# Kernel tuning notes

Hardware: AMD Instinct MI355X
Metric: run time of the kernel (lower is better)

Reference implementation:

```python
import jax, jax.numpy as jnp
import numpy as np

SIGMA_NEU = 0.05
SIGMA_SYN = 0.002
JIJ_STD = 0.045


def setup_inputs() -> dict:
    key = jax.random.key(0)
    ks = jax.random.split(key, 6)
    B, T, n_in, n_hid, n_out = 64, 64, 128, 256, 32
    input_signal = jax.random.normal(ks[0], (B, T, n_in), dtype=jnp.float32)
    hidden = jax.random.normal(ks[1], (B, n_hid), dtype=jnp.float32)
    # nn.Linear default init approximated by scaled normals; w_hh uses uniform(-jij_std, jij_std)
    w_in_w = jax.random.normal(ks[2], (n_hid, n_in), dtype=jnp.float32) / np.sqrt(n_in)
    w_hh_w = jax.random.uniform(ks[3], (n_hid, n_hid), minval=-JIJ_STD, maxval=JIJ_STD, dtype=jnp.float32)
    w_hh_b = jnp.zeros((n_hid,), dtype=jnp.float32)
    w_out_w = jax.random.normal(ks[4], (n_out, n_hid), dtype=jnp.float32) / np.sqrt(n_hid)
    alpha = jnp.full((n_hid,), 0.25, dtype=jnp.float32)
    beta = jnp.full((n_hid,), 0.1, dtype=jnp.float32)
    return {
        "input_signal": input_signal,
        "hidden": hidden,
        "length": T,
        "w_in_w": w_in_w,
        "w_hh_w": w_hh_w,
        "w_hh_b": w_hh_b,
        "w_out_w": w_out_w,
        "alpha": alpha,
        "beta": beta,
    }


def reference(input_signal, hidden, length, w_in_w, w_hh_w, w_hh_b, w_out_w, alpha, beta):
    # tanh activation, beta != 0 branch, anti-Hebbian plasticity.
    B, T, n_in = input_signal.shape
    n_hid = hidden.shape[1]
    x = jnp.transpose(input_signal, (1, 0, 2))  # (T, B, n_in)
    keys = jax.random.split(jax.random.key(42), length)
    sqrt_alpha = jnp.sqrt(alpha)
    sqrt_beta = jnp.sqrt(beta)
    # Track only different_j = new_j - w_hh (starts at 0); new_j never needed separately.
    diff_j0 = jnp.zeros((B, n_hid, n_hid), dtype=input_signal.dtype)

    def step(carry, inp):
        h, diff_j = carry
        xt, k = inp
        k1, k2 = jax.random.split(k)
        act = jnp.tanh(h)
        # row-vector times per-sample fast-weight matrix: (b,1,n) @ (b,n,n) -> (b,n)
        dj_act = jnp.einsum('bi,bij->bj', act, diff_j)
        tmp = xt @ w_in_w.T + act @ w_hh_w.T + w_hh_b + dj_act
        neural_noise = jax.random.normal(k1, h.shape, h.dtype) * SIGMA_NEU * sqrt_alpha
        h = (1.0 - alpha) * h + alpha * tmp + neural_noise
        # anti-Hebbian: -outer(act, act) + syn noise (sqrt(beta) broadcasts on last dim)
        add_w = -jnp.einsum('bi,bj->bij', act, act) \
                + jax.random.normal(k2, diff_j.shape, diff_j.dtype) * SIGMA_SYN * sqrt_beta
        diff_j = diff_j + beta * add_w
        out = 20.0 * jnp.tanh(h @ w_out_w.T)
        return (h, diff_j), (h, out)

    (hidden, _), (h_seq, o_seq) = jax.lax.scan(step, (hidden, diff_j0), (x, keys))
    hidden_list = jnp.transpose(h_seq, (1, 0, 2))  # (B, T, n_hid)
    output_list = jnp.transpose(o_seq, (1, 0, 2))  # (B, T, n_out)
    return hidden_list, output_list, hidden
```

## Files before the change

kernel.cpp:

```cpp
#include <hip/hip_runtime.h>
#include <stdint.h>

#define BB 64
#define TT 64
#define NIN 128
#define NHID 256
#define NOUT 32
#define BPS 16
#define NBLK (BB * BPS)
#define NTHR 256
#define JS 16

#define SIG_NEU 0.05f
#define SIG_SYN 0.002f

#define FLAG_OFF    0
#define FLAG_STRIDE 32
#define FLAG_BYTES  (BB * BPS * FLAG_STRIDE * 4)
#define HPUB_OFF    FLAG_BYTES

#define HID_LIST_SZ ((size_t)BB * TT * NHID)
#define OUT_LIST_SZ ((size_t)BB * TT * NOUT)

__device__ __forceinline__ uint32_t rotl32(uint32_t v, int s) {
  return __builtin_amdgcn_alignbit(v, v, 32 - s);
}

__device__ __forceinline__ void tf2x32(uint32_t k0, uint32_t k1, uint32_t x0, uint32_t x1,
                                       uint32_t& o0, uint32_t& o1) {
  const uint32_t k2 = k0 ^ k1 ^ 0x1BD11BDAu;
  x0 += k0; x1 += k1;
  x0 += x1; x1 = rotl32(x1,13); x1 ^= x0;
  x0 += x1; x1 = rotl32(x1,15); x1 ^= x0;
  x0 += x1; x1 = rotl32(x1,26); x1 ^= x0;
  x0 += x1; x1 = rotl32(x1, 6); x1 ^= x0;
  x0 += k1; x1 += k2 + 1u;
  x0 += x1; x1 = rotl32(x1,17); x1 ^= x0;
  x0 += x1; x1 = rotl32(x1,29); x1 ^= x0;
  x0 += x1; x1 = rotl32(x1,16); x1 ^= x0;
  x0 += x1; x1 = rotl32(x1,24); x1 ^= x0;
  x0 += k2; x1 += k0 + 2u;
  x0 += x1; x1 = rotl32(x1,13); x1 ^= x0;
  x0 += x1; x1 = rotl32(x1,15); x1 ^= x0;
  x0 += x1; x1 = rotl32(x1,26); x1 ^= x0;
  x0 += x1; x1 = rotl32(x1, 6); x1 ^= x0;
  x0 += k0; x1 += k1 + 3u;
  x0 += x1; x1 = rotl32(x1,17); x1 ^= x0;
  x0 += x1; x1 = rotl32(x1,29); x1 ^= x0;
  x0 += x1; x1 = rotl32(x1,16); x1 ^= x0;
  x0 += x1; x1 = rotl32(x1,24); x1 ^= x0;
  x0 += k1; x1 += k2 + 4u;
  x0 += x1; x1 = rotl32(x1,13); x1 ^= x0;
  x0 += x1; x1 = rotl32(x1,15); x1 ^= x0;
  x0 += x1; x1 = rotl32(x1,26); x1 ^= x0;
  x0 += x1; x1 = rotl32(x1, 6); x1 ^= x0;
  x0 += k2; x1 += k0 + 5u;
  o0 = x0; o1 = x1;
}

__device__ __forceinline__ float tf_normal(uint32_t k0, uint32_t k1, uint32_t idx) {
  uint32_t o0, o1;
  tf2x32(k0, k1, 0u, idx, o0, o1);
  const uint32_t bits = o0 ^ o1;
  const float u = __uint_as_float((bits >> 9) | 0x3f800000u) - 1.0f;
  float x = fmaf(u, 2.0f, -0.99999994f);
  x = fmaxf(x, -0.99999994f);
  const float w = -__logf(fmaf(-x, x, 1.0f));
  float p;
  if (w < 5.0f) {
    const float q = w - 2.5f;
    p = 2.81022636e-08f;
    p = fmaf(p, q, 3.43273939e-07f);
    p = fmaf(p, q, -3.5233877e-06f);
    p = fmaf(p, q, -4.39150654e-06f);
    p = fmaf(p, q, 0.00021858087f);
    p = fmaf(p, q, -0.00125372503f);
    p = fmaf(p, q, -0.00417768164f);
    p = fmaf(p, q, 0.246640727f);
    p = fmaf(p, q, 1.50140941f);
  } else {
    const float q = sqrtf(w) - 3.0f;
    p = -0.000200214257f;
    p = fmaf(p, q, 0.000100950558f);
    p = fmaf(p, q, 0.00134934322f);
    p = fmaf(p, q, -0.00367342844f);
    p = fmaf(p, q, 0.00573950773f);
    p = fmaf(p, q, -0.0076224613f);
    p = fmaf(p, q, 0.00943887047f);
    p = fmaf(p, q, 1.00167406f);
    p = fmaf(p, q, 2.83297682f);
  }
  return 1.41421356f * (p * x);
}

#define SPIN(slice, want)                                                         \
  do {                                                                            \
    uint32_t* fp_ = &flags[((b) * BPS + (slice)) * FLAG_STRIDE];                  \
    for (int it_ = 0; it_ < 2000000; ++it_) {                                     \
      if (__hip_atomic_load(fp_, __ATOMIC_RELAXED, __HIP_MEMORY_SCOPE_AGENT) >=   \
          (uint32_t)(want)) break;                                                \
      __builtin_amdgcn_s_sleep(1);                                                \
    }                                                                             \
  } while (0)

__global__ __launch_bounds__(NTHR, 4)
void rnn_kernel(
    const float* __restrict__ xin, const float* __restrict__ h0,
    const float* __restrict__ w_in, const float* __restrict__ w_hh,
    const float* __restrict__ b_hh, const float* __restrict__ w_out,
    const float* __restrict__ alpha, const float* __restrict__ beta,
    float* __restrict__ out, char* __restrict__ ws)
{
  __shared__ __align__(16) float whh_s[JS * 260];
  __shared__ __align__(16) float win_s[JS * 132];
  __shared__ __align__(16) float wos[2 * 260];
  __shared__ __align__(16) float h_s[NHID];
  __shared__ __align__(16) float a_s[NHID];
  __shared__ __align__(16) float xt_s[NIN];
  __shared__ float stat_s[JS];
  __shared__ float djact_s[JS];
  __shared__ uint32_t keys_s[TT * 4];

  const int tid = threadIdx.x;
  const int blk = blockIdx.x;
  const int b   = blk & 63;
  const int s   = blk >> 6;

  uint32_t* flags = (uint32_t*)(ws + FLAG_OFF);
  float*    hpub  = (float*)(ws + HPUB_OFF);

  if (tid < TT) {
    uint32_t ka, kb, t0, t1;
    tf2x32(0u, 42u, 0u, (uint32_t)tid, ka, kb);
    tf2x32(ka, kb, 0u, 0u, t0, t1);
    keys_s[tid * 4 + 0] = t0; keys_s[tid * 4 + 1] = t1;
    tf2x32(ka, kb, 0u, 1u, t0, t1);
    keys_s[tid * 4 + 2] = t0; keys_s[tid * 4 + 3] = t1;
  }
  {
    const float hv = h0[b * NHID + tid];
    h_s[tid] = hv;
    a_s[tid] = tanhf(hv);
  }
  #pragma unroll
  for (int r = 0; r < JS; ++r)
    whh_s[r * 260 + tid] = w_hh[(size_t)(s * JS + r) * NHID + tid];
  {
    const int r2 = tid >> 7, c = tid & 127;
    #pragma unroll
    for (int rr = 0; rr < 8; ++rr)
      win_s[(rr * 2 + r2) * 132 + c] = w_in[(size_t)(s * JS + rr * 2 + r2) * NIN + c];
  }
  #pragma unroll
  for (int r = 0; r < 2; ++r)
    wos[r * 260 + tid] = w_out[(s * 2 + r) * NHID + tid];

  const int q  = tid & 15;
  const int jl = tid >> 4;
  const int jg = s * JS + jl;
  const float bj   = beta[jg];
  const float sbj  = SIG_SYN * sqrtf(bj);
  const float bjsb = bj * sbj;
  const uint32_t idx0 = ((uint32_t)b << 16) | (uint32_t)jg;
  const float bias = b_hh[jg];

  uint32_t idxs[16];
  #pragma unroll
  for (int c4 = 0; c4 < 4; ++c4) {
    const uint32_t rowb = (uint32_t)(q * 16 + ((c4 + q) & 3) * 4);
    #pragma unroll
    for (int cc = 0; cc < 4; ++cc)
      idxs[c4 * 4 + cc] = idx0 + ((rowb + (uint32_t)cc) << 8);
  }

  float r_al = 0.f, r_om = 0.f, r_ns = 0.f;
  uint32_t hnidx = 0;
  if (tid < JS) {
    r_al = alpha[s * JS + tid];
    r_om = 1.0f - r_al;
    r_ns = SIG_NEU * sqrtf(r_al);
    hnidx = (uint32_t)(b * NHID + s * JS + tid);
  }

  float d[16];
  #pragma unroll
  for (int r = 0; r < 16; ++r) d[r] = 0.0f;
  float hn = 0.0f;

  __syncthreads();

  {
    if (tid < JS) {
      const uint32_t k1a = __builtin_amdgcn_readfirstlane(keys_s[0]);
      const uint32_t k1b = __builtin_amdgcn_readfirstlane(keys_s[1]);
      hn = tf_normal(k1a, k1b, hnidx);
    }
    if (tid < NIN) xt_s[tid] = xin[((size_t)b * TT) * NIN + tid];
  }
  __syncthreads();

  const int wv = tid >> 6;
  const int ln = tid & 63;

  for (int t = 0; t < TT; ++t) {
    const int par = t & 1;

    const float aj = a_s[jg];
    float pd = 0.0f;
    float acc = 0.0f;
    #pragma unroll
    for (int c4 = 0; c4 < 4; ++c4) {
      const int col = q * 16 + ((c4 + q) & 3) * 4;
      const float4 av = *(const float4*)(a_s + col);
      const float4 wv4 = *(const float4*)(whh_s + jl * 260 + col);
      pd = fmaf(av.x, d[c4*4+0], pd);
      pd = fmaf(av.y, d[c4*4+1], pd);
      pd = fmaf(av.z, d[c4*4+2], pd);
      pd = fmaf(av.w, d[c4*4+3], pd);
      d[c4*4+0] = fmaf(bj, -av.x * aj, d[c4*4+0]);
      d[c4*4+1] = fmaf(bj, -av.y * aj, d[c4*4+1]);
      d[c4*4+2] = fmaf(bj, -av.z * aj, d[c4*4+2]);
      d[c4*4+3] = fmaf(bj, -av.w * aj, d[c4*4+3]);
      acc = fmaf(wv4.x, av.x, acc); acc = fmaf(wv4.y, av.y, acc);
      acc = fmaf(wv4.z, av.z, acc); acc = fmaf(wv4.w, av.w, acc);
    }
    #pragma unroll
    for (int k = 0; k < 2; ++k) {
      const int col = q * 8 + ((k + q) & 1) * 4;
      const float4 xv = *(const float4*)(xt_s + col);
      const float4 wv4 = *(const float4*)(win_s + jl * 132 + col);
      acc = fmaf(wv4.x, xv.x, acc); acc = fmaf(wv4.y, xv.y, acc);
      acc = fmaf(wv4.z, xv.z, acc); acc = fmaf(wv4.w, xv.w, acc);
    }
    pd  += __shfl_xor(pd, 1);  pd  += __shfl_xor(pd, 2);
    pd  += __shfl_xor(pd, 4);  pd  += __shfl_xor(pd, 8);
    acc += __shfl_xor(acc, 1); acc += __shfl_xor(acc, 2);
    acc += __shfl_xor(acc, 4); acc += __shfl_xor(acc, 8);
    if (q == 0) {
      djact_s[jl] = pd;
      stat_s[jl]  = acc + bias;
    }

    if (wv == 3 && t > 0) {
      const int o = ln >> 5, sub = ln & 31;
      float oacc = 0.0f;
      #pragma unroll
      for (int k = 0; k < 2; ++k) {
        const int col = sub * 8 + ((k + sub) & 1) * 4;
        const float4 wvv = *(const float4*)(wos + o * 260 + col);
        const float4 hv  = *(const float4*)(h_s + col);
        oacc = fmaf(wvv.x, hv.x, oacc); oacc = fmaf(wvv.y, hv.y, oacc);
        oacc = fmaf(wvv.z, hv.z, oacc); oacc = fmaf(wvv.w, hv.w, oacc);
      }
      oacc += __shfl_xor(oacc, 1);  oacc += __shfl_xor(oacc, 2);
      oacc += __shfl_xor(oacc, 4);  oacc += __shfl_xor(oacc, 8);
      oacc += __shfl_xor(oacc, 16);
      if (sub == 0)
        out[HID_LIST_SZ + ((size_t)b * TT + (t - 1)) * NOUT + s * 2 + o] =
            20.0f * tanhf(oacc);
    }
    __syncthreads();

    if (tid < JS) {
      const float tmp  = stat_s[tid] + djact_s[tid];
      const float hnew = fmaf(r_al, tmp, r_om * h_s[s * JS + tid]) + hn * r_ns;
      __hip_atomic_store(&hpub[(par * BB + b) * NHID + s * JS + tid], hnew,
                         __ATOMIC_RELAXED, __HIP_MEMORY_SCOPE_AGENT);
    }
    if (tid == 0) {
      asm volatile("s_waitcnt vmcnt(0)" ::: "memory");
      __hip_atomic_store(&flags[(b * BPS + s) * FLAG_STRIDE], (uint32_t)(t + 1),
                         __ATOMIC_RELAXED, __HIP_MEMORY_SCOPE_AGENT);
    }

    if (t + 1 < TT) {
      const uint32_t k2a = __builtin_amdgcn_readfirstlane(keys_s[t * 4 + 2]);
      const uint32_t k2b = __builtin_amdgcn_readfirstlane(keys_s[t * 4 + 3]);
      #pragma unroll
      for (int e = 0; e < 16; ++e)
        d[e] = fmaf(bjsb, tf_normal(k2a, k2b, idxs[e]), d[e]);
      if (tid < JS) {
        const uint32_t k1a = __builtin_amdgcn_readfirstlane(keys_s[(t + 1) * 4 + 0]);
        const uint32_t k1b = __builtin_amdgcn_readfirstlane(keys_s[(t + 1) * 4 + 1]);
        hn = tf_normal(k1a, k1b, hnidx);
      }
    }

    if (wv == 0) {
      if (ln < BPS) SPIN(ln, t + 1);
      asm volatile("" ::: "memory");
      #pragma unroll
      for (int cc = 0; cc < 4; ++cc) {
        const int k = ln * 4 + cc;
        const float hv = __hip_atomic_load(&hpub[(par * BB + b) * NHID + k],
                                           __ATOMIC_RELAXED, __HIP_MEMORY_SCOPE_AGENT);
        h_s[k] = hv;
        a_s[k] = tanhf(hv);
      }
    } else if (wv == 1) {
      if (s == 0) {
        if (ln < BPS) SPIN(ln, t + 1);
        asm volatile("" ::: "memory");
        #pragma unroll
        for (int cc = 0; cc < 4; ++cc) {
          const int k = ln * 4 + cc;
          const float hv = __hip_atomic_load(&hpub[(par * BB + b) * NHID + k],
                                             __ATOMIC_RELAXED, __HIP_MEMORY_SCOPE_AGENT);
          out[((size_t)b * TT + t) * NHID + k] = hv;
          if (t == TT - 1)
            out[HID_LIST_SZ + OUT_LIST_SZ + (size_t)b * NHID + k] = hv;
        }
      }
    } else if (wv == 2) {
      if (t + 1 < TT) {
        xt_s[ln]      = xin[((size_t)b * TT + t + 1) * NIN + ln];
        xt_s[ln + 64] = xin[((size_t)b * TT + t + 1) * NIN + ln + 64];
      }
    }
    __syncthreads();
  }

  if (wv == 3) {
    const int o = ln >> 5, sub = ln & 31;
    float oacc = 0.0f;
    #pragma unroll
    for (int k = 0; k < 2; ++k) {
      const int col = sub * 8 + ((k + sub) & 1) * 4;
      const float4 wvv = *(const float4*)(wos + o * 260 + col);
      const float4 hv  = *(const float4*)(h_s + col);
      oacc = fmaf(wvv.x, hv.x, oacc); oacc = fmaf(wvv.y, hv.y, oacc);
      oacc = fmaf(wvv.z, hv.z, oacc); oacc = fmaf(wvv.w, hv.w, oacc);
    }
    oacc += __shfl_xor(oacc, 1);  oacc += __shfl_xor(oacc, 2);
    oacc += __shfl_xor(oacc, 4);  oacc += __shfl_xor(oacc, 8);
    oacc += __shfl_xor(oacc, 16);
    if (sub == 0)
      out[HID_LIST_SZ + ((size_t)b * TT + (TT - 1)) * NOUT + s * 2 + o] =
          20.0f * tanhf(oacc);
  }
}

extern "C" void kernel_launch(void* const* d_in, const int* in_sizes, int n_in,
                              void* d_out, int out_size, void* d_ws, size_t ws_size,
                              hipStream_t stream) {
  (void)in_sizes; (void)n_in; (void)out_size; (void)ws_size;
  const float* x     = (const float*)d_in[0];
  const float* h0    = (const float*)d_in[1];
  const float* w_in  = (const float*)d_in[3];
  const float* w_hh  = (const float*)d_in[4];
  const float* b_hh  = (const float*)d_in[5];
  const float* w_out = (const float*)d_in[6];
  const float* alpha = (const float*)d_in[7];
  const float* beta  = (const float*)d_in[8];
  float* out = (float*)d_out;

  hipMemsetAsync((char*)d_ws + FLAG_OFF, 0, FLAG_BYTES, stream);
  rnn_kernel<<<dim3(NBLK), dim3(NTHR), 0, stream>>>(
      x, h0, w_in, w_hh, b_hh, w_out, alpha, beta, out, (char*)d_ws);
}
```

Before: 816.7 us.

## Split each batch row across 32 blocks with 8 hidden units per block

Doubles the number of cooperating blocks per batch sample from 16 to 32, halving the hidden rows each block owns (JS 16→8). Each thread now holds 8 fast-weight entries instead of 16 and generates half as many synaptic-noise normals per step, with 32-lane reductions and strided float2 column access. This cuts per-block per-step compute and register pressure (launch bounds raised to 8 blocks/SM), at the cost of twice as many flags to spin on and more cross-block synchronisation traffic per timestep. The 2048 blocks must all be co-resident for the spin-wait scheme to avoid deadlock.

```diff
diff --git a/kernel.cpp b/kernel.cpp
--- a/kernel.cpp
+++ b/kernel.cpp
@@ -6,10 +6,10 @@
 #define NIN 128
 #define NHID 256
 #define NOUT 32
-#define BPS 16
+#define BPS 32
 #define NBLK (BB * BPS)
 #define NTHR 256
-#define JS 16
+#define JS 8
 
 #define SIG_NEU 0.05f
 #define SIG_SYN 0.002f
@@ -103,7 +103,7 @@
     }                                                                             \
   } while (0)
 
-__global__ __launch_bounds__(NTHR, 4)
+__global__ __launch_bounds__(NTHR, 8)
 void rnn_kernel(
     const float* __restrict__ xin, const float* __restrict__ h0,
     const float* __restrict__ w_in, const float* __restrict__ w_hh,
@@ -111,9 +111,9 @@
     const float* __restrict__ alpha, const float* __restrict__ beta,
     float* __restrict__ out, char* __restrict__ ws)
 {
-  __shared__ __align__(16) float whh_s[JS * 260];
-  __shared__ __align__(16) float win_s[JS * 132];
-  __shared__ __align__(16) float wos[2 * 260];
+  __shared__ __align__(16) float whh_s[JS * NHID];
+  __shared__ __align__(16) float win_s[JS * NIN];
+  __shared__ __align__(16) float wos_s[NHID];
   __shared__ __align__(16) float h_s[NHID];
   __shared__ __align__(16) float a_s[NHID];
   __shared__ __align__(16) float xt_s[NIN];
@@ -144,19 +144,14 @@
   }
   #pragma unroll
   for (int r = 0; r < JS; ++r)
-    whh_s[r * 260 + tid] = w_hh[(size_t)(s * JS + r) * NHID + tid];
-  {
-    const int r2 = tid >> 7, c = tid & 127;
-    #pragma unroll
-    for (int rr = 0; rr < 8; ++rr)
-      win_s[(rr * 2 + r2) * 132 + c] = w_in[(size_t)(s * JS + rr * 2 + r2) * NIN + c];
-  }
+    whh_s[r * NHID + tid] = w_hh[(size_t)(s * JS + r) * NHID + tid];
   #pragma unroll
-  for (int r = 0; r < 2; ++r)
-    wos[r * 260 + tid] = w_out[(s * 2 + r) * NHID + tid];
-
-  const int q  = tid & 15;
-  const int jl = tid >> 4;
+  for (int rr = 0; rr < 4; ++rr)
+    win_s[rr * 256 + tid] = w_in[(size_t)(s * JS) * NIN + rr * 256 + tid];
+  wos_s[tid] = w_out[s * NHID + tid];
+
+  const int q  = tid & 31;
+  const int jl = tid >> 5;
   const int jg = s * JS + jl;
   const float bj   = beta[jg];
   const float sbj  = SIG_SYN * sqrtf(bj);
@@ -164,13 +159,11 @@
   const uint32_t idx0 = ((uint32_t)b << 16) | (uint32_t)jg;
   const float bias = b_hh[jg];
 
-  uint32_t idxs[16];
+  uint32_t idxs[8];
   #pragma unroll
-  for (int c4 = 0; c4 < 4; ++c4) {
-    const uint32_t rowb = (uint32_t)(q * 16 + ((c4 + q) & 3) * 4);
-    #pragma unroll
-    for (int cc = 0; cc < 4; ++cc)
-      idxs[c4 * 4 + cc] = idx0 + ((rowb + (uint32_t)cc) << 8);
+  for (int r = 0; r < 4; ++r) {
+    idxs[2*r+0] = idx0 + ((uint32_t)(2*q + 64*r + 0) << 8);
+    idxs[2*r+1] = idx0 + ((uint32_t)(2*q + 64*r + 1) << 8);
   }
 
   float r_al = 0.f, r_om = 0.f, r_ns = 0.f;
@@ -182,9 +175,9 @@
     hnidx = (uint32_t)(b * NHID + s * JS + tid);
   }
 
-  float d[16];
+  float d[8];
   #pragma unroll
-  for (int r = 0; r < 16; ++r) d[r] = 0.0f;
+  for (int r = 0; r < 8; ++r) d[r] = 0.0f;
   float hn = 0.0f;
 
   __syncthreads();
@@ -205,59 +198,49 @@
   for (int t = 0; t < TT; ++t) {
     const int par = t & 1;
 
-    const float aj = a_s[jg];
+    const float aj   = a_s[jg];
+    const float bjaj = bj * aj;
     float pd = 0.0f;
     float acc = 0.0f;
     #pragma unroll
-    for (int c4 = 0; c4 < 4; ++c4) {
-      const int col = q * 16 + ((c4 + q) & 3) * 4;
-      const float4 av = *(const float4*)(a_s + col);
-      const float4 wv4 = *(const float4*)(whh_s + jl * 260 + col);
-      pd = fmaf(av.x, d[c4*4+0], pd);
-      pd = fmaf(av.y, d[c4*4+1], pd);
-      pd = fmaf(av.z, d[c4*4+2], pd);
-      pd = fmaf(av.w, d[c4*4+3], pd);
-      d[c4*4+0] = fmaf(bj, -av.x * aj, d[c4*4+0]);
-      d[c4*4+1] = fmaf(bj, -av.y * aj, d[c4*4+1]);
-      d[c4*4+2] = fmaf(bj, -av.z * aj, d[c4*4+2]);
-      d[c4*4+3] = fmaf(bj, -av.w * aj, d[c4*4+3]);
-      acc = fmaf(wv4.x, av.x, acc); acc = fmaf(wv4.y, av.y, acc);
-      acc = fmaf(wv4.z, av.z, acc); acc = fmaf(wv4.w, av.w, acc);
+    for (int r = 0; r < 4; ++r) {
+      const int col = 2 * q + 64 * r;
+      const float2 av = *(const float2*)(a_s + col);
+      const float2 w2 = *(const float2*)(whh_s + jl * NHID + col);
+      pd = fmaf(av.x, d[2*r+0], pd);
+      pd = fmaf(av.y, d[2*r+1], pd);
+      d[2*r+0] = fmaf(-av.x, bjaj, d[2*r+0]);
+      d[2*r+1] = fmaf(-av.y, bjaj, d[2*r+1]);
+      acc = fmaf(w2.x, av.x, acc); acc = fmaf(w2.y, av.y, acc);
     }
     #pragma unroll
-    for (int k = 0; k < 2; ++k) {
-      const int col = q * 8 + ((k + q) & 1) * 4;
-      const float4 xv = *(const float4*)(xt_s + col);
-      const float4 wv4 = *(const float4*)(win_s + jl * 132 + col);
-      acc = fmaf(wv4.x, xv.x, acc); acc = fmaf(wv4.y, xv.y, acc);
-      acc = fmaf(wv4.z, xv.z, acc); acc = fmaf(wv4.w, xv.w, acc);
+    for (int r = 0; r < 2; ++r) {
+      const int col = 2 * q + 64 * r;
+      const float2 xv = *(const float2*)(xt_s + col);
+      const float2 w2 = *(const float2*)(win_s + jl * NIN + col);
+      acc = fmaf(w2.x, xv.x, acc); acc = fmaf(w2.y, xv.y, acc);
     }
     pd  += __shfl_xor(pd, 1);  pd  += __shfl_xor(pd, 2);
     pd  += __shfl_xor(pd, 4);  pd  += __shfl_xor(pd, 8);
+    pd  += __shfl_xor(pd, 16);
     acc += __shfl_xor(acc, 1); acc += __shfl_xor(acc, 2);
     acc += __shfl_xor(acc, 4); acc += __shfl_xor(acc, 8);
+    acc += __shfl_xor(acc, 16);
     if (q == 0) {
       djact_s[jl] = pd;
       stat_s[jl]  = acc + bias;
     }
 
     if (wv == 3 && t > 0) {
-      const int o = ln >> 5, sub = ln & 31;
       float oacc = 0.0f;
       #pragma unroll
-      for (int k = 0; k < 2; ++k) {
-        const int col = sub * 8 + ((k + sub) & 1) * 4;
-        const float4 wvv = *(const float4*)(wos + o * 260 + col);
-        const float4 hv  = *(const float4*)(h_s + col);
-        oacc = fmaf(wvv.x, hv.x, oacc); oacc = fmaf(wvv.y, hv.y, oacc);
-        oacc = fmaf(wvv.z, hv.z, oacc); oacc = fmaf(wvv.w, hv.w, oacc);
-      }
+      for (int k = 0; k < 4; ++k)
+        oacc = fmaf(wos_s[ln + 64*k], h_s[ln + 64*k], oacc);
       oacc += __shfl_xor(oacc, 1);  oacc += __shfl_xor(oacc, 2);
       oacc += __shfl_xor(oacc, 4);  oacc += __shfl_xor(oacc, 8);
-      oacc += __shfl_xor(oacc, 16);
-      if (sub == 0)
-        out[HID_LIST_SZ + ((size_t)b * TT + (t - 1)) * NOUT + s * 2 + o] =
-            20.0f * tanhf(oacc);
+      oacc += __shfl_xor(oacc, 16); oacc += __shfl_xor(oacc, 32);
+      if (ln == 0)
+        out[HID_LIST_SZ + ((size_t)b * TT + (t - 1)) * NOUT + s] = 20.0f * tanhf(oacc);
     }
     __syncthreads();
 
@@ -277,7 +260,7 @@
       const uint32_t k2a = __builtin_amdgcn_readfirstlane(keys_s[t * 4 + 2]);
       const uint32_t k2b = __builtin_amdgcn_readfirstlane(keys_s[t * 4 + 3]);
       #pragma unroll
-      for (int e = 0; e < 16; ++e)
+      for (int e = 0; e < 8; ++e)
         d[e] = fmaf(bjsb, tf_normal(k2a, k2b, idxs[e]), d[e]);
       if (tid < JS) {
         const uint32_t k1a = __builtin_amdgcn_readfirstlane(keys_s[(t + 1) * 4 + 0]);
@@ -291,7 +274,7 @@
       asm volatile("" ::: "memory");
       #pragma unroll
       for (int cc = 0; cc < 4; ++cc) {
-        const int k = ln * 4 + cc;
+        const int k = ln + 64 * cc;
         const float hv = __hip_atomic_load(&hpub[(par * BB + b) * NHID + k],
                                            __ATOMIC_RELAXED, __HIP_MEMORY_SCOPE_AGENT);
         h_s[k] = hv;
@@ -303,7 +286,7 @@
         asm volatile("" ::: "memory");
         #pragma unroll
         for (int cc = 0; cc < 4; ++cc) {
-          const int k = ln * 4 + cc;
+          const int k = ln + 64 * cc;
           const float hv = __hip_atomic_load(&hpub[(par * BB + b) * NHID + k],
                                              __ATOMIC_RELAXED, __HIP_MEMORY_SCOPE_AGENT);
           out[((size_t)b * TT + t) * NHID + k] = hv;
@@ -321,22 +304,15 @@
   }
 
   if (wv == 3) {
-    const int o = ln >> 5, sub = ln & 31;
     float oacc = 0.0f;
     #pragma unroll
-    for (int k = 0; k < 2; ++k) {
-      const int col = sub * 8 + ((k + sub) & 1) * 4;
-      const float4 wvv = *(const float4*)(wos + o * 260 + col);
-      const float4 hv  = *(const float4*)(h_s + col);
-      oacc = fmaf(wvv.x, hv.x, oacc); oacc = fmaf(wvv.y, hv.y, oacc);
-      oacc = fmaf(wvv.z, hv.z, oacc); oacc = fmaf(wvv.w, hv.w, oacc);
-    }
+    for (int k = 0; k < 4; ++k)
+      oacc = fmaf(wos_s[ln + 64*k], h_s[ln + 64*k], oacc);
     oacc += __shfl_xor(oacc, 1);  oacc += __shfl_xor(oacc, 2);
     oacc += __shfl_xor(oacc, 4);  oacc += __shfl_xor(oacc, 8);
-    oacc += __shfl_xor(oacc, 16);
-    if (sub == 0)
-      out[HID_LIST_SZ + ((size_t)b * TT + (TT - 1)) * NOUT + s * 2 + o] =
-          20.0f * tanhf(oacc);
+    oacc += __shfl_xor(oacc, 16); oacc += __shfl_xor(oacc, 32);
+    if (ln == 0)
+      out[HID_LIST_SZ + ((size_t)b * TT + (TT - 1)) * NOUT + s] = 20.0f * tanhf(oacc);
   }
 }
 
```

New measurement: 893.5 us. 9.4% more time.
